# Kernel tuning notes

Hardware: AMD Instinct MI355X
Metric: run time of the kernel (lower is better)

## Reference

```python
import jax, jax.numpy as jnp
import numpy as np

NUM_HEADS = 12
EPS = 1e-6


def _rms_norm(x, w):
    # RMSNorm over the full channel dim (applied before head split), fp32 math
    return x * jax.lax.rsqrt(jnp.mean(x * x, axis=-1, keepdims=True) + EPS) * w


def _rope_apply(t, F, H, W, freqs):
    # t: [B, S, n, d] with S == F*H*W; freqs: [1024, d//2] angles
    B, S, n, d = t.shape
    c = d // 2
    s0 = c - 2 * (c // 3)  # temporal split (22 when d=128)
    s1 = c // 3            # spatial splits (21, 21)
    f0, f1, f2 = freqs[:, :s0], freqs[:, s0:s0 + s1], freqs[:, s0 + s1:]
    ang = jnp.concatenate([
        jnp.broadcast_to(f0[:F, None, None, :], (F, H, W, s0)),
        jnp.broadcast_to(f1[None, :H, None, :], (F, H, W, s1)),
        jnp.broadcast_to(f2[None, None, :W, :], (F, H, W, s1)),
    ], axis=-1).reshape(S, c)                      # [S, c]
    cos = jnp.cos(ang)[None, :, None, :]           # [1, S, 1, c]
    sin = jnp.sin(ang)[None, :, None, :]
    tp = t.reshape(B, S, n, c, 2)
    te, to = tp[..., 0], tp[..., 1]                # complex (real, imag) pairs
    rot = jnp.stack([te * cos - to * sin, te * sin + to * cos], axis=-1)
    return rot.reshape(B, S, n, d)


def reference(x, seq_lens, grid_sizes, freqs, Wq, bq, Wk, bk, Wv, bv, Wo, bo, norm_q_w, norm_k_w):
    B, S, C = x.shape
    n = NUM_HEADS
    d = C // n
    gs = np.asarray(grid_sizes)[0]
    F, H, W = int(gs[0]), int(gs[1]), int(gs[2])  # static: L == F*H*W, same per sample

    q = _rms_norm(x @ Wq.T + bq, norm_q_w).reshape(B, S, n, d)
    k = _rms_norm(x @ Wk.T + bk, norm_k_w).reshape(B, S, n, d)
    v = (x @ Wv.T + bv).reshape(B, S, n, d)

    q = _rope_apply(q, F, H, W, freqs)
    k = _rope_apply(k, F, H, W, freqs)

    scale = 1.0 / jnp.sqrt(jnp.float32(d))
    scores = jnp.einsum('bqnd,bknd->bnqk', q, k) * scale   # [B, n, S, S]
    kmask = jnp.arange(S)[None, :] < seq_lens[:, None]      # [B, S] valid keys
    scores = jnp.where(kmask[:, None, None, :], scores, -jnp.inf)
    attn = jax.nn.softmax(scores, axis=-1)
    out = jnp.einsum('bnqk,bknd->bqnd', attn, v).reshape(B, S, C)
    return out @ Wo.T + bo


def setup_inputs() -> dict:
    key = jax.random.key(0)
    ks = jax.random.split(key, 10)
    B, F, H, W = 2, 4, 24, 32
    S = F * H * W  # 3072
    C = 1536
    d = C // NUM_HEADS  # 128
    c = d // 2          # 64

    x = jax.random.normal(ks[0], (B, S, C), dtype=jnp.float32)
    seq_lens = jnp.array([S, 2500], dtype=jnp.int32)
    grid_sizes = jnp.array([[F, H, W]] * B, dtype=jnp.int32)

    # rope angles: outer(pos, 1/theta^(2i/dim)) per split [22, 21, 21]
    def rope_params(max_len, dim_k, theta=10000.0):
        inv = 1.0 / (theta ** (np.arange(0, dim_k, 2, dtype=np.float64) / dim_k))
        return np.outer(np.arange(max_len), inv)
    s0 = c - 2 * (c // 3)
    s1 = c // 3
    freqs = jnp.asarray(np.concatenate([
        rope_params(1024, 2 * s0), rope_params(1024, 2 * s1), rope_params(1024, 2 * s1)
    ], axis=1), dtype=jnp.float32)  # [1024, 64]

    std = 0.02
    def lin(k):
        return jax.random.normal(k, (C, C), dtype=jnp.float32) * std
    return {
        'x': x, 'seq_lens': seq_lens, 'grid_sizes': grid_sizes, 'freqs': freqs,
        'Wq': lin(ks[1]), 'bq': jnp.zeros((C,), jnp.float32),
        'Wk': lin(ks[2]), 'bk': jnp.zeros((C,), jnp.float32),
        'Wv': lin(ks[3]), 'bv': jnp.zeros((C,), jnp.float32),
        'Wo': lin(ks[4]), 'bo': jnp.zeros((C,), jnp.float32),
        'norm_q_w': jnp.ones((C,), jnp.float32),
        'norm_k_w': jnp.ones((C,), jnp.float32),
    }
```

## Files before the change

### kernel.cpp

```cpp
#include <hip/hip_runtime.h>
#include <hip/hip_bf16.h>
#include <math.h>

#define NB 2
#define SS 3072
#define CC 1536
#define NH 12
#define DH 128
#define NTOK (NB * SS)
#define WE (CC * CC)
#define LOG2E 1.4426950408889634f

typedef __attribute__((ext_vector_type(8))) short short8;
typedef __attribute__((ext_vector_type(4))) float floatx4;

#define GLOAD(g, l) __builtin_amdgcn_global_load_lds( \
    (const __attribute__((address_space(1))) void*)(g), \
    (__attribute__((address_space(3))) void*)(l), 16, 0, 0)

__device__ __forceinline__ unsigned short f2bf(float f) {
    unsigned u = __float_as_uint(f);
    u += 0x7fffu + ((u >> 16) & 1u);
    return (unsigned short)(u >> 16);
}
__device__ __forceinline__ int swz(int row, int q) {
    return row * 4 + (q ^ ((row >> 1) & 3));
}

__global__ __launch_bounds__(256) void cast_all(
    const float* __restrict__ x,
    const float* __restrict__ w0, const float* __restrict__ w1,
    const float* __restrict__ w2, const float* __restrict__ w3,
    unsigned short* __restrict__ o)
{
    const int y = blockIdx.y;
    const float* src = (y < 4) ? x + (size_t)y * WE
                     : (y == 4) ? w0 : (y == 5) ? w1 : (y == 6) ? w2 : w3;
    size_t i = ((size_t)blockIdx.x * 256 + threadIdx.x) * 4;
    float4 v = *(const float4*)&src[i];
    uint2 u;
    u.x = (unsigned)f2bf(v.x) | ((unsigned)f2bf(v.y) << 16);
    u.y = (unsigned)f2bf(v.z) | ((unsigned)f2bf(v.w) << 16);
    *(uint2*)&o[(size_t)y * WE + i] = u;
}

__global__ __launch_bounds__(256) void rope_table(
    const float* __restrict__ freqs, const int* __restrict__ gsz,
    float2* __restrict__ tab)
{
    const int id = blockIdx.x * 256 + threadIdx.x;
    const int s = id >> 6, pj = id & 63;
    const int Hg = gsz[1], Wg = gsz[2];
    const int f = s / (Hg * Wg);
    const int rem = s - f * Hg * Wg;
    const int hh = rem / Wg;
    const int ww = rem - hh * Wg;
    const int row = (pj < 22) ? f : ((pj < 43) ? hh : ww);
    float sn, cs;
    sincosf(freqs[row * 64 + pj], &sn, &cs);
    tab[id] = make_float2(cs, sn);
}

__global__ __launch_bounds__(256) void qkv_gemm(
    const unsigned short* __restrict__ X,
    const unsigned short* __restrict__ Wqb, const unsigned short* __restrict__ Wkb,
    const unsigned short* __restrict__ Wvb,
    const float* __restrict__ bq, const float* __restrict__ bk,
    const float* __restrict__ bv,
    unsigned short* __restrict__ qo, unsigned short* __restrict__ ko,
    unsigned short* __restrict__ vto)
{
    __shared__ unsigned short As[128 * 32];
    __shared__ unsigned short Bs[128 * 32];
    const int tid = threadIdx.x;
    const int w = tid >> 6, l = tid & 63;
    const int jseg = blockIdx.y / 12;
    const unsigned short* Wt = (jseg == 0) ? Wqb : (jseg == 1) ? Wkb : Wvb;
    const float* bias        = (jseg == 0) ? bq  : (jseg == 1) ? bk  : bv;
    unsigned short* Y        = (jseg == 0) ? qo  : (jseg == 1) ? ko  : vto;
    const int i0 = blockIdx.x * 128, j0 = (blockIdx.y % 12) * 128;
    const int srow = tid >> 2;
    const int gk8 = (((tid & 3) ^ ((srow >> 1) & 3))) * 8;

    floatx4 acc[4][4] = {};
    for (int k0 = 0; k0 < CC; k0 += 32) {
        __syncthreads();
        GLOAD(X + (size_t)(i0 + srow) * CC + k0 + gk8,        As + (size_t)tid * 8);
        GLOAD(X + (size_t)(i0 + 64 + srow) * CC + k0 + gk8,   As + (size_t)(256 + tid) * 8);
        GLOAD(Wt + (size_t)(j0 + srow) * CC + k0 + gk8,       Bs + (size_t)tid * 8);
        GLOAD(Wt + (size_t)(j0 + 64 + srow) * CC + k0 + gk8,  Bs + (size_t)(256 + tid) * 8);
        __syncthreads();
        const int wr = (w >> 1) * 64, wc = (w & 1) * 64;
        short8 af[4], bf[4];
        #pragma unroll
        for (int mb = 0; mb < 4; ++mb)
            af[mb] = *(const short8*)&As[swz(wr + mb * 16 + (l & 15), l >> 4) * 8];
        #pragma unroll
        for (int nb = 0; nb < 4; ++nb)
            bf[nb] = *(const short8*)&Bs[swz(wc + nb * 16 + (l & 15), l >> 4) * 8];
        #pragma unroll
        for (int mb = 0; mb < 4; ++mb)
            #pragma unroll
            for (int nb = 0; nb < 4; ++nb)
                acc[mb][nb] = __builtin_amdgcn_mfma_f32_16x16x32_bf16(
                    af[mb], bf[nb], acc[mb][nb], 0, 0, 0);
    }

    const int wr = (w >> 1) * 64, wc = (w & 1) * 64;
    #pragma unroll
    for (int mb = 0; mb < 4; ++mb)
        #pragma unroll
        for (int nb = 0; nb < 4; ++nb) {
            const int n = j0 + wc + nb * 16 + (l & 15);
            const float bv2 = bias[n];
            const int h = n >> 7, td = n & 127;
            #pragma unroll
            for (int r = 0; r < 4; ++r) {
                const int m = i0 + wr + mb * 16 + (l >> 4) * 4 + r;
                const float val = acc[mb][nb][r] + bv2;
                const int b = (m >= SS) ? 1 : 0;
                const int s = m - b * SS;
                if (jseg < 2)
                    Y[((size_t)(b * NH + h) * SS + s) * DH + td] = f2bf(val);
                else
                    Y[((size_t)(b * NH + h) * DH + td) * SS + s] = f2bf(val);
            }
        }
}

__global__ __launch_bounds__(256) void gemm_o(
    const unsigned short* __restrict__ X, const unsigned short* __restrict__ Wt,
    const float* __restrict__ bias, float* __restrict__ Y)
{
    __shared__ unsigned short As[128 * 32];
    __shared__ unsigned short Bs[128 * 32];
    const int tid = threadIdx.x;
    const int w = tid >> 6, l = tid & 63;
    const int i0 = blockIdx.x * 128, j0 = blockIdx.y * 128;
    const int srow = tid >> 2;
    const int gk8 = (((tid & 3) ^ ((srow >> 1) & 3))) * 8;

    floatx4 acc[4][4] = {};
    for (int k0 = 0; k0 < CC; k0 += 32) {
        __syncthreads();
        GLOAD(X + (size_t)(i0 + srow) * CC + k0 + gk8,        As + (size_t)tid * 8);
        GLOAD(X + (size_t)(i0 + 64 + srow) * CC + k0 + gk8,   As + (size_t)(256 + tid) * 8);
        GLOAD(Wt + (size_t)(j0 + srow) * CC + k0 + gk8,       Bs + (size_t)tid * 8);
        GLOAD(Wt + (size_t)(j0 + 64 + srow) * CC + k0 + gk8,  Bs + (size_t)(256 + tid) * 8);
        __syncthreads();
        const int wr = (w >> 1) * 64, wc = (w & 1) * 64;
        short8 af[4], bf[4];
        #pragma unroll
        for (int mb = 0; mb < 4; ++mb)
            af[mb] = *(const short8*)&As[swz(wr + mb * 16 + (l & 15), l >> 4) * 8];
        #pragma unroll
        for (int nb = 0; nb < 4; ++nb)
            bf[nb] = *(const short8*)&Bs[swz(wc + nb * 16 + (l & 15), l >> 4) * 8];
        #pragma unroll
        for (int mb = 0; mb < 4; ++mb)
            #pragma unroll
            for (int nb = 0; nb < 4; ++nb)
                acc[mb][nb] = __builtin_amdgcn_mfma_f32_16x16x32_bf16(
                    af[mb], bf[nb], acc[mb][nb], 0, 0, 0);
    }

    const int wr = (w >> 1) * 64, wc = (w & 1) * 64;
    #pragma unroll
    for (int mb = 0; mb < 4; ++mb)
        #pragma unroll
        for (int nb = 0; nb < 4; ++nb) {
            const int n = j0 + wc + nb * 16 + (l & 15);
            const float bv = bias[n];
            #pragma unroll
            for (int r = 0; r < 4; ++r) {
                const int m = i0 + wr + mb * 16 + (l >> 4) * 4 + r;
                Y[(size_t)m * CC + n] = acc[mb][nb][r] + bv;
            }
        }
}

__global__ __launch_bounds__(256) void norm_rope(
    unsigned short* __restrict__ qb, unsigned short* __restrict__ kb,
    const float* __restrict__ nqw, const float* __restrict__ nkw,
    const float2* __restrict__ tab)
{
    const int bid = blockIdx.x;
    const int which = (bid >= NTOK) ? 1 : 0;
    const int tok = bid - which * NTOK;
    unsigned short* t    = which ? kb : qb;
    const float* wgt     = which ? nkw : nqw;
    const float outscale = which ? 1.0f : 0.08838834764831845f * LOG2E;
    const int b = tok / SS, s = tok - b * SS;
    const int tid = threadIdx.x;

    float2 vals[3];
    size_t addrs[3];
    float ss = 0.f;
    #pragma unroll
    for (int kt = 0; kt < 3; ++kt) {
        int p = tid + kt * 256;
        int h = p >> 6, pj = p & 63;
        size_t addr = ((size_t)(b * NH + h) * SS + s) * DH + 2 * pj;
        addrs[kt] = addr;
        unsigned u = *(const unsigned*)&t[addr];
        float2 v;
        v.x = __uint_as_float(u << 16);
        v.y = __uint_as_float(u & 0xffff0000u);
        vals[kt] = v;
        ss += v.x * v.x + v.y * v.y;
    }
    #pragma unroll
    for (int off = 32; off > 0; off >>= 1) ss += __shfl_down(ss, off, 64);
    __shared__ float red[4];
    if ((tid & 63) == 0) red[tid >> 6] = ss;
    __syncthreads();
    const float total = red[0] + red[1] + red[2] + red[3];
    const float rstd = rsqrtf(total * (1.0f / CC) + 1e-6f) * outscale;

    #pragma unroll
    for (int kt = 0; kt < 3; ++kt) {
        int p = tid + kt * 256;
        int h = p >> 6, pj = p & 63;
        float2 cssn = tab[s * 64 + pj];
        int ch = h * DH + 2 * pj;
        float te = vals[kt].x * rstd * wgt[ch];
        float to = vals[kt].y * rstd * wgt[ch + 1];
        unsigned o = (unsigned)f2bf(te * cssn.x - to * cssn.y) |
                     ((unsigned)f2bf(te * cssn.y + to * cssn.x) << 16);
        *(unsigned*)&t[addrs[kt]] = o;
    }
}

__global__ __launch_bounds__(256, 2) void flash_attn_mfma(
    const unsigned short* __restrict__ qg, const unsigned short* __restrict__ kg,
    const unsigned short* __restrict__ vg, const int* __restrict__ seq_lens,
    unsigned short* __restrict__ out)
{
    __shared__ unsigned short lds[37376];
    const int tid = threadIdx.x;
    const int w = tid >> 6, l = tid & 63;
    unsigned short* Psw = lds + 32768 + w * (16 * 72);

    const int bid = blockIdx.x;
    const int qt = bid / (NB * NH);
    const int rem0 = bid - qt * (NB * NH);
    const int h = rem0 >> 1;
    const int b = rem0 & 1;
    const int slen = seq_lens[b];
    const int s0 = qt * 128;

    const unsigned short* qbase = qg + ((size_t)(b * NH + h) * SS + s0) * DH;
    const unsigned short* kbase = kg + ((size_t)(b * NH + h) * SS) * DH;
    const unsigned short* vbase = vg + ((size_t)(b * NH + h) * DH) * SS;

    #pragma unroll
    for (int i = 0; i < 8; ++i) {
        int cid = i * 256 + tid;
        int kc = cid >> 9, r2 = cid & 511, row = r2 >> 2, sq = r2 & 3;
        GLOAD(qbase + (size_t)row * DH + kc * 32 + (sq ^ ((row >> 1) & 3)) * 8,
              lds + (size_t)cid * 8);
    }
    __syncthreads();
    short8 qf[2][4];
    #pragma unroll
    for (int rb = 0; rb < 2; ++rb)
        #pragma unroll
        for (int kc = 0; kc < 4; ++kc)
            qf[rb][kc] = *(const short8*)&lds[(kc * 512 + swz(w * 32 + rb * 16 + (l & 15), l >> 4)) * 8];
    __syncthreads();

    int ksrc[4], vsrc[4];
    #pragma unroll
    for (int i = 0; i < 4; ++i) {
        int cid = i * 256 + tid;
        {   int kc = cid >> 8, r2 = cid & 255, row = r2 >> 2, sq = r2 & 3;
            ksrc[i] = row * DH + kc * 32 + (sq ^ ((row >> 1) & 3)) * 8; }
        {   int ks = cid >> 9, r2 = cid & 511, dc = r2 >> 2, sq = r2 & 3;
            vsrc[i] = dc * SS + ks * 32 + (sq ^ ((dc >> 1) & 3)) * 8; }
    }

    const int ntiles = (slen + 63) >> 6;

    #pragma unroll
    for (int i = 0; i < 4; ++i) {
        int cid = i * 256 + tid;
        GLOAD(kbase + ksrc[i],        lds + (size_t)cid * 8);
        GLOAD(vbase + vsrc[i],        lds + 8192 + (size_t)cid * 8);
    }

    floatx4 acc[2][8] = {};
    float lsum[2][4] = {};

    for (int kt = 0; kt < ntiles; ++kt) {
        __syncthreads();

        if (kt + 1 < ntiles) {
            const unsigned short* kb2 = kbase + (size_t)(kt + 1) * 64 * DH;
            const unsigned short* vb2 = vbase + (size_t)(kt + 1) * 64;
            unsigned short* dst = lds + ((kt + 1) & 1) * 16384;
            #pragma unroll
            for (int i = 0; i < 4; ++i) {
                int cid = i * 256 + tid;
                GLOAD(kb2 + ksrc[i], dst + (size_t)cid * 8);
                GLOAD(vb2 + vsrc[i], dst + 8192 + (size_t)cid * 8);
            }
        }

        const unsigned short* Ks = lds + (kt & 1) * 16384;
        const unsigned short* Vs = Ks + 8192;

        floatx4 sv[2][4] = {};
        #pragma unroll
        for (int kc = 0; kc < 4; ++kc) {
            short8 kf[4];
            #pragma unroll
            for (int nb = 0; nb < 4; ++nb)
                kf[nb] = *(const short8*)&Ks[(kc * 256 + swz(nb * 16 + (l & 15), l >> 4)) * 8];
            #pragma unroll
            for (int rb = 0; rb < 2; ++rb)
                #pragma unroll
                for (int nb = 0; nb < 4; ++nb)
                    sv[rb][nb] = __builtin_amdgcn_mfma_f32_16x16x32_bf16(
                        qf[rb][kc], kf[nb], sv[rb][nb], 0, 0, 0);
        }

        const int valid = slen - kt * 64;
        short8 pa[2][2];
        #pragma unroll
        for (int rb = 0; rb < 2; ++rb) {
            if (valid >= 64) {
                #pragma unroll
                for (int nb = 0; nb < 4; ++nb)
                    #pragma unroll
                    for (int r = 0; r < 4; ++r)
                        sv[rb][nb][r] = exp2f(sv[rb][nb][r]);
            } else {
                #pragma unroll
                for (int nb = 0; nb < 4; ++nb) {
                    const int key = nb * 16 + (l & 15);
                    #pragma unroll
                    for (int r = 0; r < 4; ++r)
                        sv[rb][nb][r] = (key < valid) ? exp2f(sv[rb][nb][r]) : 0.0f;
                }
            }
            #pragma unroll
            for (int r = 0; r < 4; ++r)
                lsum[rb][r] += sv[rb][0][r] + sv[rb][1][r] + sv[rb][2][r] + sv[rb][3][r];
            #pragma unroll
            for (int nb = 0; nb < 4; ++nb)
                #pragma unroll
                for (int r = 0; r < 4; r += 2) {
                    union { __hip_bfloat162 v; ushort2 u; } cv;
                    cv.v = __float22bfloat162_rn(
                        make_float2(sv[rb][nb][r], sv[rb][nb][r + 1]));
                    const int rowb = (l >> 4) * 4 + r;
                    Psw[rowb * 72 + nb * 16 + (l & 15)]       = cv.u.x;
                    Psw[(rowb + 1) * 72 + nb * 16 + (l & 15)] = cv.u.y;
                }
            #pragma unroll
            for (int ks = 0; ks < 2; ++ks)
                pa[rb][ks] = *(const short8*)&Psw[(l & 15) * 72 + ks * 32 + (l >> 4) * 8];
        }

        #pragma unroll
        for (int ks = 0; ks < 2; ++ks)
            #pragma unroll
            for (int nb2 = 0; nb2 < 8; ++nb2) {
                short8 vf = *(const short8*)&Vs[(ks * 512 + swz(nb2 * 16 + (l & 15), l >> 4)) * 8];
                #pragma unroll
                for (int rb = 0; rb < 2; ++rb)
                    acc[rb][nb2] = __builtin_amdgcn_mfma_f32_16x16x32_bf16(
                        pa[rb][ks], vf, acc[rb][nb2], 0, 0, 0);
            }
    }

    #pragma unroll
    for (int rb = 0; rb < 2; ++rb) {
        float rl[4];
        #pragma unroll
        for (int r = 0; r < 4; ++r) {
            float s = lsum[rb][r];
            #pragma unroll
            for (int mm = 1; mm < 16; mm <<= 1) s += __shfl_xor(s, mm, 64);
            rl[r] = 1.0f / s;
        }
        #pragma unroll
        for (int nb2 = 0; nb2 < 8; ++nb2) {
            const int col = h * DH + nb2 * 16 + (l & 15);
            #pragma unroll
            for (int r = 0; r < 4; ++r) {
                const int srow = s0 + w * 32 + rb * 16 + (l >> 4) * 4 + r;
                out[((size_t)b * SS + srow) * CC + col] = f2bf(acc[rb][nb2][r] * rl[r]);
            }
        }
    }
}

extern "C" void kernel_launch(void* const* d_in, const int* in_sizes, int n_in,
                              void* d_out, int out_size, void* d_ws, size_t ws_size,
                              hipStream_t stream) {
    const float* x          = (const float*)d_in[0];
    const int*   seq_lens   = (const int*)d_in[1];
    const int*   grid_sizes = (const int*)d_in[2];
    const float* freqs      = (const float*)d_in[3];
    const float* Wq         = (const float*)d_in[4];
    const float* bq         = (const float*)d_in[5];
    const float* Wk         = (const float*)d_in[6];
    const float* bk         = (const float*)d_in[7];
    const float* Wv         = (const float*)d_in[8];
    const float* bv         = (const float*)d_in[9];
    const float* Wo         = (const float*)d_in[10];
    const float* bo         = (const float*)d_in[11];
    const float* nqw        = (const float*)d_in[12];
    const float* nkw        = (const float*)d_in[13];
    float* out = (float*)d_out;

    const size_t TE = (size_t)NTOK * CC;
    unsigned short* xb  = (unsigned short*)d_ws;
    unsigned short* wqb = xb + TE;
    unsigned short* wkb = wqb + WE;
    unsigned short* wvb = wkb + WE;
    unsigned short* wob = wvb + WE;
    unsigned short* qb  = wob + WE;
    unsigned short* kb  = qb + TE;
    unsigned short* vtb = kb + TE;
    unsigned short* ab  = vtb + TE;
    float2* tab = (float2*)(ab + TE);

    cast_all<<<dim3(WE / 1024, 8), 256, 0, stream>>>(x, Wq, Wk, Wv, Wo, xb);
    rope_table<<<dim3(SS * 64 / 256), 256, 0, stream>>>(freqs, grid_sizes, tab);

    qkv_gemm<<<dim3(NTOK / 128, 36), 256, 0, stream>>>(
        xb, wqb, wkb, wvb, bq, bk, bv, qb, kb, vtb);

    norm_rope<<<dim3(2 * NTOK), 256, 0, stream>>>(qb, kb, nqw, nkw, tab);

    flash_attn_mfma<<<dim3(NB * NH * (SS / 128)), 256, 0, stream>>>(qb, kb, vtb, seq_lens, ab);

    gemm_o<<<dim3(NTOK / 128, CC / 128), 256, 0, stream>>>(ab, wob, bo, out);
}
```

Measured before the change: 525.2 us.

## Compute S transposed and build P fragments with permlane swaps instead of LDS

The QK^T MFMA operands are swapped so each lane holds scores for one query row across keys. The P operand for the PV MFMA can then be assembled in registers with v_permlane32/16_swap instead of a round trip through LDS. This removes the per-wave P scratch area in shared memory, and with it LDS writes, reads and bank traffic. Row sums are now reduced across lanes differently. s_setprio is also raised around the MFMA blocks to favour matrix issue. The risk is that the lane-permutation mapping must exactly match the MFMA operand layout.

After: 519.1 us. No clear change (-1.2%).

```diff
diff --git a/kernel.cpp b/kernel.cpp
--- a/kernel.cpp
+++ b/kernel.cpp
@@ -236,10 +236,9 @@
     const unsigned short* __restrict__ vg, const int* __restrict__ seq_lens,
     unsigned short* __restrict__ out)
 {
-    __shared__ unsigned short lds[37376];
+    __shared__ unsigned short lds[32768];
     const int tid = threadIdx.x;
     const int w = tid >> 6, l = tid & 63;
-    unsigned short* Psw = lds + 32768 + w * (16 * 72);
 
     const int bid = blockIdx.x;
     const int qt = bid / (NB * NH);
@@ -289,7 +288,8 @@
     }
 
     floatx4 acc[2][8] = {};
-    float lsum[2][4] = {};
+    float lsum[2] = {};
+    const int g4 = (l >> 4) * 4;
 
     for (int kt = 0; kt < ntiles; ++kt) {
         __syncthreads();
@@ -310,6 +310,7 @@
         const unsigned short* Vs = Ks + 8192;
 
         floatx4 sv[2][4] = {};
+        __builtin_amdgcn_s_setprio(1);
         #pragma unroll
         for (int kc = 0; kc < 4; ++kc) {
             short8 kf[4];
@@ -321,8 +322,9 @@
                 #pragma unroll
                 for (int nb = 0; nb < 4; ++nb)
                     sv[rb][nb] = __builtin_amdgcn_mfma_f32_16x16x32_bf16(
-                        qf[rb][kc], kf[nb], sv[rb][nb], 0, 0, 0);
-        }
+                        kf[nb], qf[rb][kc], sv[rb][nb], 0, 0, 0);
+        }
+        __builtin_amdgcn_s_setprio(0);
 
         const int valid = slen - kt * 64;
         short8 pa[2][2];
@@ -336,32 +338,42 @@
                         sv[rb][nb][r] = exp2f(sv[rb][nb][r]);
             } else {
                 #pragma unroll
-                for (int nb = 0; nb < 4; ++nb) {
-                    const int key = nb * 16 + (l & 15);
+                for (int nb = 0; nb < 4; ++nb)
                     #pragma unroll
-                    for (int r = 0; r < 4; ++r)
+                    for (int r = 0; r < 4; ++r) {
+                        const int key = g4 + r + 16 * nb;
                         sv[rb][nb][r] = (key < valid) ? exp2f(sv[rb][nb][r]) : 0.0f;
-                }
-            }
-            #pragma unroll
-            for (int r = 0; r < 4; ++r)
-                lsum[rb][r] += sv[rb][0][r] + sv[rb][1][r] + sv[rb][2][r] + sv[rb][3][r];
+                    }
+            }
             #pragma unroll
             for (int nb = 0; nb < 4; ++nb)
-                #pragma unroll
-                for (int r = 0; r < 4; r += 2) {
-                    union { __hip_bfloat162 v; ushort2 u; } cv;
-                    cv.v = __float22bfloat162_rn(
-                        make_float2(sv[rb][nb][r], sv[rb][nb][r + 1]));
-                    const int rowb = (l >> 4) * 4 + r;
-                    Psw[rowb * 72 + nb * 16 + (l & 15)]       = cv.u.x;
-                    Psw[(rowb + 1) * 72 + nb * 16 + (l & 15)] = cv.u.y;
-                }
-            #pragma unroll
-            for (int ks = 0; ks < 2; ++ks)
-                pa[rb][ks] = *(const short8*)&Psw[(l & 15) * 72 + ks * 32 + (l >> 4) * 8];
-        }
-
+                lsum[rb] += (sv[rb][nb][0] + sv[rb][nb][1]) +
+                            (sv[rb][nb][2] + sv[rb][nb][3]);
+
+            unsigned dw0[4], dw1[4];
+            #pragma unroll
+            for (int nb = 0; nb < 4; ++nb) {
+                union { __hip_bfloat162 v; unsigned u; } c0, c1;
+                c0.v = __float22bfloat162_rn(make_float2(sv[rb][nb][0], sv[rb][nb][1]));
+                c1.v = __float22bfloat162_rn(make_float2(sv[rb][nb][2], sv[rb][nb][3]));
+                dw0[nb] = c0.u;
+                dw1[nb] = c1.u;
+            }
+            #pragma unroll
+            for (int ks = 0; ks < 2; ++ks) {
+                unsigned x0 = dw0[2 * ks], y0 = dw0[2 * ks + 1];
+                unsigned x1 = dw1[2 * ks], y1 = dw1[2 * ks + 1];
+                asm("v_permlane32_swap_b32 %0, %1" : "+v"(x0), "+v"(y0));
+                asm("v_permlane16_swap_b32 %0, %1" : "+v"(x0), "+v"(y0));
+                asm("v_permlane32_swap_b32 %0, %1" : "+v"(x1), "+v"(y1));
+                asm("v_permlane16_swap_b32 %0, %1" : "+v"(x1), "+v"(y1));
+                union { short8 s; unsigned u[4]; } pk;
+                pk.u[0] = x0; pk.u[1] = x1; pk.u[2] = y0; pk.u[3] = y1;
+                pa[rb][ks] = pk.s;
+            }
+        }
+
+        __builtin_amdgcn_s_setprio(1);
         #pragma unroll
         for (int ks = 0; ks < 2; ++ks)
             #pragma unroll
@@ -372,18 +384,18 @@
                     acc[rb][nb2] = __builtin_amdgcn_mfma_f32_16x16x32_bf16(
                         pa[rb][ks], vf, acc[rb][nb2], 0, 0, 0);
             }
+        __builtin_amdgcn_s_setprio(0);
     }
 
     #pragma unroll
     for (int rb = 0; rb < 2; ++rb) {
+        float s = lsum[rb];
+        s += __shfl_xor(s, 16, 64);
+        s += __shfl_xor(s, 32, 64);
         float rl[4];
         #pragma unroll
-        for (int r = 0; r < 4; ++r) {
-            float s = lsum[rb][r];
-            #pragma unroll
-            for (int mm = 1; mm < 16; mm <<= 1) s += __shfl_xor(s, mm, 64);
-            rl[r] = 1.0f / s;
-        }
+        for (int r = 0; r < 4; ++r)
+            rl[r] = 1.0f / __shfl(s, g4 + r, 64);
         #pragma unroll
         for (int nb2 = 0; nb2 < 8; ++nb2) {
             const int col = h * DH + nb2 * 16 + (l & 15);
```
